# Performance work log

Measured on AMD Instinct MI355X. Metric: run time of the kernel, lower is better.

## Reference

```python
import jax, jax.numpy as jnp
import numpy as np

D_MODEL = 1024
POOL = 2048
K = 16
D_FF = 4096
N_HEADS = 16
TEMP = 1.0
EPS = 1e-5


def _ln(x, g, b):
    mu = jnp.mean(x, axis=-1, keepdims=True)
    var = jnp.mean((x - mu) ** 2, axis=-1, keepdims=True)
    return (x - mu) * jax.lax.rsqrt(var + EPS) * g + b


def setup_inputs() -> dict:
    key = jax.random.key(0)
    ks = jax.random.split(key, 12)
    s = 0.02
    return {
        "x": jax.random.normal(ks[0], (4, 1024, D_MODEL), jnp.float32),
        "w_router": s * jax.random.normal(ks[1], (D_MODEL, POOL), jnp.float32),
        "b_router": jnp.zeros((POOL,), jnp.float32),
        "firing": s * jax.random.normal(ks[2], (POOL, D_FF), jnp.float32),
        "w_pool_out": s * jax.random.normal(ks[3], (D_FF, D_MODEL), jnp.float32),
        "b_pool_out": jnp.zeros((D_MODEL,), jnp.float32),
        "w_in": s * jax.random.normal(ks[4], (D_MODEL, 3 * D_MODEL), jnp.float32),
        "b_in": jnp.zeros((3 * D_MODEL,), jnp.float32),
        "w_attn_out": s * jax.random.normal(ks[5], (D_MODEL, D_MODEL), jnp.float32),
        "b_attn_out": jnp.zeros((D_MODEL,), jnp.float32),
        "g1": jnp.ones((D_MODEL,), jnp.float32),
        "beta1": jnp.zeros((D_MODEL,), jnp.float32),
        "g2": jnp.ones((D_MODEL,), jnp.float32),
        "beta2": jnp.zeros((D_MODEL,), jnp.float32),
    }


def reference(x, w_router, b_router, firing, w_pool_out, b_pool_out,
              w_in, b_in, w_attn_out, b_attn_out, g1, beta1, g2, beta2):
    B, S, D = x.shape
    Hd = D // N_HEADS
    # --- Context router: score every neuron, select top-k, softmax weights ---
    scores = x @ w_router + b_router                      # [B,S,P]
    top_vals, top_idx = jax.lax.top_k(scores, K)          # [B,S,K]
    weights = jax.nn.softmax(top_vals / TEMP, axis=-1)    # [B,S,K]
    # --- Neuron pool: gather firing patterns, weighted combine, GELU, project ---
    patterns = firing[top_idx]                            # [B,S,K,d_ff] gather
    combined = jnp.einsum('bsk,bskf->bsf', weights, patterns)  # [B,S,d_ff]
    neuron_out = jax.nn.gelu(combined, approximate=False) @ w_pool_out + b_pool_out  # [B,S,D]
    # --- Self-attention over neuron_out (dropout inactive at eval) ---
    qkv = neuron_out @ w_in + b_in                        # [B,S,3D]
    q, k, v = jnp.split(qkv, 3, axis=-1)
    q = q.reshape(B, S, N_HEADS, Hd).transpose(0, 2, 1, 3)
    k = k.reshape(B, S, N_HEADS, Hd).transpose(0, 2, 1, 3)
    v = v.reshape(B, S, N_HEADS, Hd).transpose(0, 2, 1, 3)
    logits = jnp.einsum('bhqd,bhkd->bhqk', q, k) / jnp.sqrt(jnp.float32(Hd))
    probs = jax.nn.softmax(logits, axis=-1)
    ctx = jnp.einsum('bhqk,bhkd->bhqd', probs, v)
    ctx = ctx.transpose(0, 2, 1, 3).reshape(B, S, D)
    attn_out = ctx @ w_attn_out + b_attn_out
    # --- Residuals + norms ---
    h = _ln(x + attn_out, g1, beta1)
    out = _ln(h + neuron_out, g2, beta2)
    return out
```

## Files before the change

kernel.cpp:

```cpp
#include <hip/hip_runtime.h>
#include <math.h>

typedef __attribute__((ext_vector_type(8))) __bf16 bf16x8;
typedef __attribute__((ext_vector_type(4))) __bf16 bf16x4;
typedef __attribute__((ext_vector_type(4))) float f32x4;

#define DEV static __device__ __forceinline__

DEV float b2f(unsigned short u){ union{unsigned i; float f;} c; c.i=((unsigned)u)<<16; return c.f; }
DEV unsigned short f2b(float f){
  union{float f; unsigned u;} c; c.f=f;
  unsigned r = 0x7FFFu + ((c.u>>16)&1u);
  return (unsigned short)((c.u + r)>>16);
}
DEV unsigned pack2(float a, float b){ return (unsigned)f2b(a) | ((unsigned)f2b(b)<<16); }
DEV float gelu_exact(float x){ return 0.5f*x*(1.f+erff(x*0.70710678118654752f)); }

typedef __attribute__((address_space(1))) void gas_void;
typedef __attribute__((address_space(3))) void las_void;
DEV void gload_lds16(const unsigned short* g, unsigned short* l){
  __builtin_amdgcn_global_load_lds((const gas_void*)g, (las_void*)l, 16, 0, 0);
}

template<int N> DEV void waitcnt_vm(){
  if constexpr(N==0)      asm volatile("s_waitcnt vmcnt(0)" ::: "memory");
  else if constexpr(N==2) asm volatile("s_waitcnt vmcnt(2)" ::: "memory");
  else if constexpr(N==3) asm volatile("s_waitcnt vmcnt(3)" ::: "memory");
  else if constexpr(N==4) asm volatile("s_waitcnt vmcnt(4)" ::: "memory");
  else if constexpr(N==6) asm volatile("s_waitcnt vmcnt(6)" ::: "memory");
  else if constexpr(N==8) asm volatile("s_waitcnt vmcnt(8)" ::: "memory");
  else                    asm volatile("s_waitcnt vmcnt(0)" ::: "memory");
}

__global__ __launch_bounds__(256) void k_cast_bf16(const float* __restrict__ in,
                                                   unsigned short* __restrict__ out, long n4)
{
  long i = (long)blockIdx.x*256 + threadIdx.x;
  if (i >= n4) return;
  float4 v = ((const float4*)in)[i];
  ushort4 o; o.x=f2b(v.x); o.y=f2b(v.y); o.z=f2b(v.z); o.w=f2b(v.w);
  ((ushort4*)out)[i] = o;
}

__global__ __launch_bounds__(256) void k_transpose_cast(const float* __restrict__ in,
                                                        unsigned short* __restrict__ out,
                                                        int R, int C)
{
  __shared__ float tile[32][33];
  const int tc = blockIdx.x*32, tr = blockIdx.y*32;
  {
    const int r = threadIdx.x>>3, c4 = (threadIdx.x&7)*4;
    float4 v = *(const float4*)&in[(long)(tr+r)*C + tc+c4];
    tile[r][c4+0]=v.x; tile[r][c4+1]=v.y; tile[r][c4+2]=v.z; tile[r][c4+3]=v.w;
  }
  __syncthreads();
  {
    const int c = threadIdx.x>>3, r4 = (threadIdx.x&7)*4;
    ushort4 o;
    o.x = f2b(tile[r4+0][c]); o.y = f2b(tile[r4+1][c]);
    o.z = f2b(tile[r4+2][c]); o.w = f2b(tile[r4+3][c]);
    *(ushort4*)&out[(long)(tc+c)*R + tr+r4] = o;
  }
}

template<int WR, int WC, int FM, int FN, int OMODE>
__global__ __launch_bounds__(WR*WC*64, 2) void k_gemm_bt(
  const unsigned short* __restrict__ A, long lda, long sAb,
  const unsigned short* __restrict__ Bt, long ldb, long sBb,
  float* __restrict__ Cf, unsigned short* __restrict__ Cb, long ldc, long sCb,
  const float* __restrict__ bias, int Kiters)
{
  constexpr int WAVES = WR*WC;
  constexpr int BM = WR*FM*16, BN = WC*FN*16;
  constexpr int AR16 = BM/16, TOT16 = (BM+BN)/16;
  constexpr int UNITS = TOT16/WAVES;
  static_assert(TOT16 % WAVES == 0, "stage units must split across waves");
  __shared__ __align__(16) unsigned short S[3][TOT16*512];
  const int tid = threadIdx.x;
  const int wave = tid>>6, lane = tid&63;
  const int wr = wave/WC, wc = wave%WC;
  const int l15 = lane&15, lhi = lane>>4;
  const int lrow = lane>>2;
  const int lcol = ((lane&3) ^ ((lrow>>1)&3))*8;

  const int gx = gridDim.x;
  const int nwg = gx*gridDim.y;
  const int id = blockIdx.y*gx + blockIdx.x;
  const int sid = (id&7)*(nwg>>3) + (id>>3);
  const long bm = (long)(sid / gx)*BM, bn = (long)(sid % gx)*BN;

  const unsigned short* Ab  = A  + (long)blockIdx.z*sAb + bm*lda;
  const unsigned short* Btb = Bt + (long)blockIdx.z*sBb + bn*ldb;

  f32x4 acc[FM][FN];
  #pragma unroll
  for (int i=0;i<FM;i++)
    #pragma unroll
    for (int j=0;j<FN;j++) acc[i][j] = (f32x4){0.f,0.f,0.f,0.f};

  auto STAGE = [&](int kt, int buf){
    const long k0 = (long)kt*32;
    #pragma unroll
    for (int u=0; u<UNITS; ++u) {
      const int t = wave + u*WAVES;
      const unsigned short* g;
      if (t < AR16) g = Ab  + (long)(t*16 + lrow)*lda + k0 + lcol;
      else          g = Btb + (long)((t-AR16)*16 + lrow)*ldb + k0 + lcol;
      gload_lds16(g, &S[buf][t*512]);
    }
  };
  auto COMPUTE = [&](int buf){
    const unsigned short* Sb = S[buf];
    bf16x8 bfr[FN];
    #pragma unroll
    for (int j=0;j<FN;j++) {
      const int r = wc*(FN*16) + j*16 + l15;
      bfr[j] = *(const bf16x8*)&Sb[BM*32 + r*32 + ((lhi ^ ((r>>1)&3))*8)];
    }
    #pragma unroll
    for (int i=0;i<FM;i++) {
      const int r = wr*(FM*16) + i*16 + l15;
      bf16x8 a = *(const bf16x8*)&Sb[r*32 + ((lhi ^ ((r>>1)&3))*8)];
      #pragma unroll
      for (int j=0;j<FN;j++)
        acc[i][j] = __builtin_amdgcn_mfma_f32_16x16x32_bf16(a, bfr[j], acc[i][j], 0,0,0);
    }
  };

  STAGE(0, 0);
  if (Kiters > 1) STAGE(1, 1);
  for (int kt=0; kt<Kiters; ++kt) {
    if (kt+1 < Kiters) waitcnt_vm<UNITS>();
    else               waitcnt_vm<0>();
    __builtin_amdgcn_s_barrier();
    __builtin_amdgcn_sched_barrier(0);
    COMPUTE(kt%3);
    if (kt+2 < Kiters) STAGE(kt+2, (kt+2)%3);
  }

  #pragma unroll
  for (int i=0;i<FM;i++) {
    #pragma unroll
    for (int j=0;j<FN;j++) {
      long col = bn + wc*(FN*16) + j*16 + l15;
      float bb = bias ? bias[col] : 0.f;
      #pragma unroll
      for (int q=0;q<4;q++) {
        long row = bm + wr*(FM*16) + i*16 + lhi*4 + q;
        float v = acc[i][j][q] + bb;
        long off = (long)blockIdx.z*sCb + row*ldc + col;
        if constexpr (OMODE==0 || OMODE==2) Cf[off] = v;
        if constexpr (OMODE==1 || OMODE==2) Cb[off] = f2b(v);
      }
    }
  }
}

__global__ __launch_bounds__(256) void k_combine_bias_bf16(
    const float* __restrict__ p, long sz, const float* __restrict__ bias,
    unsigned short* __restrict__ outb)
{
  const long t = blockIdx.x;
  const int tid = threadIdx.x;
  float4 a = ((const float4*)(p + t*1024))[tid];
  float4 b = ((const float4*)(p + sz + t*1024))[tid];
  float4 bi = ((const float4*)bias)[tid];
  ushort4 o;
  o.x = f2b(a.x+b.x+bi.x); o.y = f2b(a.y+b.y+bi.y);
  o.z = f2b(a.z+b.z+bi.z); o.w = f2b(a.w+b.w+bi.w);
  ((ushort4*)(outb + t*1024))[tid] = o;
}

__global__ __launch_bounds__(256) void k_topk_softmax(const float* __restrict__ scores,
                                                      int* __restrict__ topidx,
                                                      float* __restrict__ topw)
{
  const int tid = threadIdx.x, wave = tid>>6, lane = tid&63;
  const long t = blockIdx.x;
  const float* row = scores + t*2048;
  const int base = wave*512 + lane*8;
  unsigned k0,k1,k2,k3,k4,k5,k6,k7;
  {
    float4 a = *(const float4*)(row + base);
    float4 b = *(const float4*)(row + base + 4);
    float v[8] = {a.x,a.y,a.z,a.w,b.x,b.y,b.z,b.w};
    unsigned kk[8];
    #pragma unroll
    for (int e=0;e<8;e++){
      int bi = __float_as_int(v[e]);
      unsigned u = (bi<0) ? ~(unsigned)bi : ((unsigned)bi | 0x80000000u);
      kk[e] = (u & 0xFFFFF800u) | (unsigned)(2047 - (base+e));
    }
    k0=kk[0];k1=kk[1];k2=kk[2];k3=kk[3];k4=kk[4];k5=kk[5];k6=kk[6];k7=kk[7];
  }
  #define CX(x,y) { unsigned mx = x>y?x:y, mn = x>y?y:x; x=mx; y=mn; }
  CX(k0,k1) CX(k2,k3) CX(k4,k5) CX(k6,k7)
  CX(k0,k2) CX(k1,k3) CX(k4,k6) CX(k5,k7)
  CX(k1,k2) CX(k5,k6)
  CX(k0,k4) CX(k1,k5) CX(k2,k6) CX(k3,k7)
  CX(k2,k4) CX(k3,k5)
  CX(k1,k2) CX(k3,k4) CX(k5,k6)
  #undef CX

  __shared__ unsigned wk[4][16];
  unsigned my1 = 0;
  for (int it=0; it<16; ++it){
    unsigned best = k0;
    #pragma unroll
    for (int off=1; off<64; off<<=1){
      unsigned o = __shfl_xor(best, off);
      best = o>best ? o : best;
    }
    if (lane==it) my1 = best;
    bool own = (k0==best);
    k0 = own?k1:k0; k1 = own?k2:k1; k2 = own?k3:k2; k3 = own?k4:k3;
    k4 = own?k5:k4; k5 = own?k6:k5; k6 = own?k7:k6; k7 = own?0u:k7;
  }
  if (lane < 16) wk[wave][lane] = my1;
  __syncthreads();
  if (wave == 0){
    unsigned c = wk[lane>>4][lane&15];
    unsigned my2 = 0;
    for (int it=0; it<16; ++it){
      unsigned best = c;
      #pragma unroll
      for (int off=1; off<64; off<<=1){
        unsigned o = __shfl_xor(best, off);
        best = o>best ? o : best;
      }
      if (lane==it) my2 = best;
      c = (c==best) ? 0u : c;
    }
    int idx = 2047 - (int)(my2 & 0x7FFu);
    float val = -1e30f;
    if (lane < 16) val = row[idx];
    float m0 = __shfl(val, 0);
    float e = (lane < 16) ? __expf(val - m0) : 0.f;
    float s = e;
    #pragma unroll
    for (int off=1; off<64; off<<=1) s += __shfl_xor(s, off);
    if (lane < 16){
      topw[t*16+lane]   = e/s;
      topidx[t*16+lane] = idx;
    }
  }
}

__global__ __launch_bounds__(256) void k_gather_gelu(const int* __restrict__ topidx,
                                                     const float* __restrict__ topw,
                                                     const unsigned short* __restrict__ firing,
                                                     unsigned short* __restrict__ gact)
{
  __shared__ int idx[4][16]; __shared__ float w[4][16];
  const int tid = threadIdx.x;
  const int c = blockIdx.x & 7;
  const long t0 = (long)(blockIdx.x >> 3) * 4;
  if (tid < 64) {
    int tok = tid >> 4, k = tid & 15;
    idx[tok][k] = topidx[(t0+tok)*16 + k];
    w[tok][k]   = topw[(t0+tok)*16 + k];
  }
  __syncthreads();
  const int tok = tid >> 6, lane = tid & 63;
  const int f0 = c*512 + lane*8;
  float acc[8] = {0,0,0,0,0,0,0,0};
  #pragma unroll
  for (int k=0;k<16;k++) {
    uint4 v = *(const uint4*)(firing + (long)idx[tok][k]*4096 + f0);
    const unsigned short* pu = (const unsigned short*)&v;
    float wk = w[tok][k];
    #pragma unroll
    for (int e=0;e<8;e++) acc[e] += wk * b2f(pu[e]);
  }
  float g[8];
  #pragma unroll
  for (int e=0;e<8;e++) g[e] = gelu_exact(acc[e]);
  uint4 ov;
  ov.x = pack2(g[0],g[1]); ov.y = pack2(g[2],g[3]);
  ov.z = pack2(g[4],g[5]); ov.w = pack2(g[6],g[7]);
  *(uint4*)(gact + (t0+tok)*4096 + f0) = ov;
}

__global__ __launch_bounds__(256) void k_vtrans(const unsigned short* __restrict__ qkv,
                                                unsigned short* __restrict__ vT)
{
  __shared__ unsigned short tile[64][65];
  int bh = blockIdx.y; int b = bh>>4, h = bh&15;
  long t0 = (long)blockIdx.x*64;
  const int tid = threadIdx.x;
  #pragma unroll
  for (int s=0;s<16;s++) {
    int i = tid + s*256;
    int r = i>>6, c = i&63;
    tile[r][c] = qkv[ (long)(b*1024 + t0 + r)*3072 + 2048 + h*64 + c ];
  }
  __syncthreads();
  #pragma unroll
  for (int s=0;s<16;s++) {
    int i = tid + s*256;
    int c = i>>6, r = i&63;
    vT[ (long)bh*65536 + (long)c*1024 + t0 + r ] = tile[r][c];
  }
}

__global__ __launch_bounds__(256) void k_flash_attn(
  const unsigned short* __restrict__ qkv,
  const unsigned short* __restrict__ vT,
  unsigned short* __restrict__ ctx)
{
  __shared__ __align__(16) unsigned short Ks[2][128*64];
  __shared__ __align__(16) unsigned short Vs[2][64*128];
  const int tid = threadIdx.x;
  const int wave = tid>>6, lane = tid&63;
  const int l15 = lane&15, lhi = lane>>4;
  const int bh = blockIdx.x, b = bh>>4, h = bh&15;
  const long q0 = (long)blockIdx.y*128;
  const unsigned short* Qg = qkv + ((long)b*1024 + q0)*3072 + h*64;
  const unsigned short* Kg = qkv + (long)b*1024*3072 + 1024 + h*64;
  const unsigned short* Vg = vT + (long)bh*65536;

  auto STAGE_KV = [&](int t, int s){
    const long kv0 = (long)t*128;
    const int sr = lane>>3, sc = (lane&7)^sr;
    #pragma unroll
    for (int uu=0; uu<4; ++uu){
      int u = wave + uu*4;
      gload_lds16(Kg + (kv0 + u*8 + sr)*3072 + sc*8, &Ks[s][u*512]);
    }
    const int vc = (lane&15) ^ ((wave&1)*4 + lhi);
    #pragma unroll
    for (int uu=0; uu<4; ++uu){
      int u = wave + uu*4;
      gload_lds16(Vg + (long)(u*4+lhi)*1024 + kv0 + vc*8, &Vs[s][u*512]);
    }
  };

  STAGE_KV(0, 0);

  bf16x8 qf[2][2];
  #pragma unroll
  for (int jq=0;jq<2;jq++){
    const long r = wave*32 + jq*16 + l15;
    #pragma unroll
    for (int ks=0;ks<2;ks++)
      qf[jq][ks] = *(const bf16x8*)(Qg + r*3072 + ks*32 + lhi*8);
  }
  __syncthreads();

  f32x4 acco[2][4];
  #pragma unroll
  for (int mi=0;mi<2;mi++)
    #pragma unroll
    for (int nf=0;nf<4;nf++) acco[mi][nf] = (f32x4){0.f,0.f,0.f,0.f};
  float m_run[2] = {-1e30f,-1e30f}, l_run[2] = {0.f,0.f};

  int sel = 0;
  for (int t=0; t<8; ++t) {
    if (t < 7) STAGE_KV(t+1, sel^1);
    f32x4 accs[8][2];
    #pragma unroll
    for (int fk=0;fk<8;fk++){
      accs[fk][0] = (f32x4){0.f,0.f,0.f,0.f};
      accs[fk][1] = (f32x4){0.f,0.f,0.f,0.f};
      const int r = fk*16 + l15;
      bf16x8 k0 = *(const bf16x8*)&Ks[sel][r*64 + ((lhi^(r&7))*8)];
      accs[fk][0] = __builtin_amdgcn_mfma_f32_16x16x32_bf16(k0, qf[0][0], accs[fk][0],0,0,0);
      accs[fk][1] = __builtin_amdgcn_mfma_f32_16x16x32_bf16(k0, qf[1][0], accs[fk][1],0,0,0);
      bf16x8 k1 = *(const bf16x8*)&Ks[sel][r*64 + (((4+lhi)^(r&7))*8)];
      accs[fk][0] = __builtin_amdgcn_mfma_f32_16x16x32_bf16(k1, qf[0][1], accs[fk][0],0,0,0);
      accs[fk][1] = __builtin_amdgcn_mfma_f32_16x16x32_bf16(k1, qf[1][1], accs[fk][1],0,0,0);
    }
    bf16x8 pa[2][4];
    float fsc[2];
    #pragma unroll
    for (int jq=0;jq<2;jq++){
      float mt = -1e30f;
      #pragma unroll
      for (int fk=0;fk<8;fk++)
        #pragma unroll
        for (int q=0;q<4;q++) mt = fmaxf(mt, accs[fk][jq][q]);
      mt = fmaxf(mt, __shfl_xor(mt,16));
      mt = fmaxf(mt, __shfl_xor(mt,32));
      mt *= 0.125f;
      float mnew = fmaxf(m_run[jq], mt);
      float fj = __expf(m_run[jq] - mnew);
      float ssum = 0.f;
      #pragma unroll
      for (int fk=0;fk<8;fk++)
        #pragma unroll
        for (int q=0;q<4;q++){
          float p = __expf(accs[fk][jq][q]*0.125f - mnew);
          ssum += p;
          pa[jq][fk>>1][(fk&1)*4+q] = (__bf16)p;
        }
      ssum += __shfl_xor(ssum,16);
      ssum += __shfl_xor(ssum,32);
      l_run[jq] = l_run[jq]*fj + ssum;
      m_run[jq] = mnew;
      fsc[jq] = fj;
    }
    #pragma unroll
    for (int mi=0;mi<2;mi++)
      #pragma unroll
      for (int q=0;q<4;q++){
        float fr = __shfl(fsc[mi], (lane&48)|(lhi*4+q));
        #pragma unroll
        for (int nf=0;nf<4;nf++) acco[mi][nf][q] *= fr;
      }
    #pragma unroll
    for (int kk=0;kk<4;kk++)
      #pragma unroll
      for (int nf=0;nf<4;nf++){
        const int rv = nf*16 + l15;
        const int cb = kk*4 + (lhi>>1);
        bf16x4 v0 = *(const bf16x4*)&Vs[sel][rv*128 + (( cb   ^(l15&7))*8) + (lhi&1)*4];
        bf16x4 v1 = *(const bf16x4*)&Vs[sel][rv*128 + (((cb+2)^(l15&7))*8) + (lhi&1)*4];
        bf16x8 vb = __builtin_shufflevector(v0, v1, 0,1,2,3,4,5,6,7);
        acco[0][nf] = __builtin_amdgcn_mfma_f32_16x16x32_bf16(pa[0][kk], vb, acco[0][nf],0,0,0);
        acco[1][nf] = __builtin_amdgcn_mfma_f32_16x16x32_bf16(pa[1][kk], vb, acco[1][nf],0,0,0);
      }
    __syncthreads();
    sel ^= 1;
  }

  #pragma unroll
  for (int mi=0;mi<2;mi++)
    #pragma unroll
    for (int q=0;q<4;q++){
      float lr = __shfl(l_run[mi], (lane&48)|(lhi*4+q));
      float inv = 1.f/lr;
      long row = q0 + wave*32 + mi*16 + lhi*4 + q;
      #pragma unroll
      for (int nf=0;nf<4;nf++)
        ctx[((long)b*1024 + row)*1024 + h*64 + nf*16 + l15] = f2b(acco[mi][nf][q]*inv);
    }
}

__global__ __launch_bounds__(256) void k_ln_res_fb(const float* __restrict__ a,
                                                   const unsigned short* __restrict__ b,
                                                   const float* __restrict__ g,
                                                   const float* __restrict__ be,
                                                   float* __restrict__ out)
{
  const long t = blockIdx.x;
  const int tid = threadIdx.x;
  const int wave = tid>>6, lane = tid&63;
  float4 av = ((const float4*)(a + t*1024))[tid];
  ushort4 ub = ((const ushort4*)(b + t*1024))[tid];
  float4 sv = { av.x + b2f(ub.x), av.y + b2f(ub.y),
                av.z + b2f(ub.z), av.w + b2f(ub.w) };
  float sum = sv.x+sv.y+sv.z+sv.w;
  float sq  = sv.x*sv.x + sv.y*sv.y + sv.z*sv.z + sv.w*sv.w;
  #pragma unroll
  for (int off=32; off; off>>=1){ sum += __shfl_xor(sum,off); sq += __shfl_xor(sq,off); }
  __shared__ float s1[4], s2[4];
  if (lane==0){ s1[wave]=sum; s2[wave]=sq; }
  __syncthreads();
  sum = s1[0]+s1[1]+s1[2]+s1[3];
  sq  = s2[0]+s2[1]+s2[2]+s2[3];
  float mu  = sum * (1.f/1024.f);
  float var = sq * (1.f/1024.f) - mu*mu;
  float rs  = rsqrtf(var + 1e-5f);
  float4 gv  = ((const float4*)g)[tid];
  float4 bev = ((const float4*)be)[tid];
  float4 ov = { (sv.x-mu)*rs*gv.x + bev.x,
                (sv.y-mu)*rs*gv.y + bev.y,
                (sv.z-mu)*rs*gv.z + bev.z,
                (sv.w-mu)*rs*gv.w + bev.w };
  ((float4*)(out + t*1024))[tid] = ov;
}

extern "C" void kernel_launch(void* const* d_in, const int* in_sizes, int n_in,
                              void* d_out, int out_size, void* d_ws, size_t ws_size,
                              hipStream_t stream)
{
  const float* x        = (const float*)d_in[0];
  const float* w_router = (const float*)d_in[1];
  const float* b_router = (const float*)d_in[2];
  const float* firing   = (const float*)d_in[3];
  const float* w_pool   = (const float*)d_in[4];
  const float* b_pool   = (const float*)d_in[5];
  const float* w_in     = (const float*)d_in[6];
  const float* b_in     = (const float*)d_in[7];
  const float* w_ao     = (const float*)d_in[8];
  const float* b_ao     = (const float*)d_in[9];
  const float* g1       = (const float*)d_in[10];
  const float* be1      = (const float*)d_in[11];
  const float* g2       = (const float*)d_in[12];
  const float* be2      = (const float*)d_in[13];
  float* out = (float*)d_out;
  char* ws = (char*)d_ws;

  unsigned short* xb    = (unsigned short*)(ws + 0);
  unsigned short* wrT   = (unsigned short*)(ws + 8388608);
  unsigned short* firb  = (unsigned short*)(ws + 12582912);
  unsigned short* wpoT  = (unsigned short*)(ws + 29360128);
  unsigned short* winT  = (unsigned short*)(ws + 37748736);
  unsigned short* waoT  = (unsigned short*)(ws + 44040192);
  float*  scores        = (float*)(ws + 46137344);
  unsigned short* gact  = (unsigned short*)(ws + 46137344);
  int*    topi          = (int*)(ws + 79691776);
  float*  topw          = (float*)(ws + 79953920);
  unsigned short* attnb = (unsigned short*)(ws + 80216064);
  unsigned short* neub  = (unsigned short*)(ws + 96993280);
  unsigned short* qkvb  = (unsigned short*)(ws + 105381888);
  unsigned short* vT    = (unsigned short*)(ws + 130547712);
  unsigned short* ctx   = (unsigned short*)(ws + 138936320);
  float*  hbuf          = (float*)(ws + 147324928);
  float*  poolp         = (float*)(ws + 130547712);

  if (ws_size < 164102144u) return;

  k_cast_bf16<<<4096, 256, 0, stream>>>(x, xb, 4096L*1024/4);
  k_cast_bf16<<<8192, 256, 0, stream>>>(firing, firb, 2048L*4096/4);
  k_transpose_cast<<<dim3(2048/32, 1024/32), 256, 0, stream>>>(w_router, wrT, 1024, 2048);
  k_transpose_cast<<<dim3(1024/32, 4096/32), 256, 0, stream>>>(w_pool,   wpoT, 4096, 1024);
  k_transpose_cast<<<dim3(3072/32, 1024/32), 256, 0, stream>>>(w_in,     winT, 1024, 3072);
  k_transpose_cast<<<dim3(1024/32, 1024/32), 256, 0, stream>>>(w_ao,     waoT, 1024, 1024);

  k_gemm_bt<2,2,4,4,0><<<dim3(16,32,1),256,0,stream>>>(xb,1024,0, wrT,1024,0,
        scores,nullptr,2048,0, b_router, 32);
  k_topk_softmax<<<4096,256,0,stream>>>(scores, topi, topw);
  k_gather_gelu<<<8192,256,0,stream>>>(topi, topw, firb, gact);

  k_gemm_bt<2,2,4,4,0><<<dim3(8,32,2),256,0,stream>>>(gact,4096,2048, wpoT,4096,2048,
        poolp,nullptr,1024,4194304, nullptr, 64);
  k_combine_bias_bf16<<<4096,256,0,stream>>>(poolp, 4194304, b_pool, neub);

  k_gemm_bt<2,2,4,4,1><<<dim3(24,32,1),256,0,stream>>>(neub,1024,0, winT,1024,0,
        nullptr,qkvb,3072,0, b_in, 32);

  k_vtrans<<<dim3(16,64),256,0,stream>>>(qkvb, vT);
  k_flash_attn<<<dim3(64,8),256,0,stream>>>(qkvb, vT, ctx);

  k_gemm_bt<2,2,4,2,1><<<dim3(16,32,1),256,0,stream>>>(ctx,1024,0, waoT,1024,0,
        nullptr,attnb,1024,0, b_ao, 32);

  k_ln_res_fb<<<4096,256,0,stream>>>(x, attnb, g1, be1, hbuf);
  k_ln_res_fb<<<4096,256,0,stream>>>(hbuf, neub, g2, be2, out);
}
```

Measured before the change: 275.1 us.

## Use 8 waves per flash-attention block with lazy softmax rescaling

Flash attention now runs 512 threads per block, so each wave owns 16 query rows instead of 32, which halves per-thread accumulators and register pressure and raises occupancy. K/V staging is split across 8 waves. Online softmax now skips the max update and accumulator rescale unless the new tile max exceeds the running max by more than 8 (in the scaled log domain). This is the FlashAttention-4 style conditional rescale, which stays exact after final normalisation but allows unnormalised probabilities up to about e^8 in bf16/fp32. Each K/V tile loaded into LDS is now reused by fewer query rows per wave, though still by 128 query rows per block.

After: 271.8 us. About the same (-1.2%).

```diff
diff --git a/kernel.cpp b/kernel.cpp
--- a/kernel.cpp
+++ b/kernel.cpp
@@ -303,7 +303,7 @@
   }
 }
 
-__global__ __launch_bounds__(256) void k_flash_attn(
+__global__ __launch_bounds__(512, 4) void k_flash_attn(
   const unsigned short* __restrict__ qkv,
   const unsigned short* __restrict__ vT,
   unsigned short* __restrict__ ctx)
@@ -323,90 +323,79 @@
     const long kv0 = (long)t*128;
     const int sr = lane>>3, sc = (lane&7)^sr;
     #pragma unroll
-    for (int uu=0; uu<4; ++uu){
-      int u = wave + uu*4;
+    for (int uu=0; uu<2; ++uu){
+      int u = wave + uu*8;
       gload_lds16(Kg + (kv0 + u*8 + sr)*3072 + sc*8, &Ks[s][u*512]);
     }
     const int vc = (lane&15) ^ ((wave&1)*4 + lhi);
     #pragma unroll
-    for (int uu=0; uu<4; ++uu){
-      int u = wave + uu*4;
+    for (int uu=0; uu<2; ++uu){
+      int u = wave + uu*8;
       gload_lds16(Vg + (long)(u*4+lhi)*1024 + kv0 + vc*8, &Vs[s][u*512]);
     }
   };
 
   STAGE_KV(0, 0);
 
-  bf16x8 qf[2][2];
-  #pragma unroll
-  for (int jq=0;jq<2;jq++){
-    const long r = wave*32 + jq*16 + l15;
-    #pragma unroll
-    for (int ks=0;ks<2;ks++)
-      qf[jq][ks] = *(const bf16x8*)(Qg + r*3072 + ks*32 + lhi*8);
+  bf16x8 qf[2];
+  {
+    const long r = wave*16 + l15;
+    qf[0] = *(const bf16x8*)(Qg + r*3072 + lhi*8);
+    qf[1] = *(const bf16x8*)(Qg + r*3072 + 32 + lhi*8);
   }
   __syncthreads();
 
-  f32x4 acco[2][4];
-  #pragma unroll
-  for (int mi=0;mi<2;mi++)
-    #pragma unroll
-    for (int nf=0;nf<4;nf++) acco[mi][nf] = (f32x4){0.f,0.f,0.f,0.f};
-  float m_run[2] = {-1e30f,-1e30f}, l_run[2] = {0.f,0.f};
+  f32x4 acco[4];
+  #pragma unroll
+  for (int nf=0;nf<4;nf++) acco[nf] = (f32x4){0.f,0.f,0.f,0.f};
+  float m_run = -1e30f, l_run = 0.f;
 
   int sel = 0;
   for (int t=0; t<8; ++t) {
     if (t < 7) STAGE_KV(t+1, sel^1);
-    f32x4 accs[8][2];
+    f32x4 accs[8];
     #pragma unroll
     for (int fk=0;fk<8;fk++){
-      accs[fk][0] = (f32x4){0.f,0.f,0.f,0.f};
-      accs[fk][1] = (f32x4){0.f,0.f,0.f,0.f};
+      accs[fk] = (f32x4){0.f,0.f,0.f,0.f};
       const int r = fk*16 + l15;
       bf16x8 k0 = *(const bf16x8*)&Ks[sel][r*64 + ((lhi^(r&7))*8)];
-      accs[fk][0] = __builtin_amdgcn_mfma_f32_16x16x32_bf16(k0, qf[0][0], accs[fk][0],0,0,0);
-      accs[fk][1] = __builtin_amdgcn_mfma_f32_16x16x32_bf16(k0, qf[1][0], accs[fk][1],0,0,0);
+      accs[fk] = __builtin_amdgcn_mfma_f32_16x16x32_bf16(k0, qf[0], accs[fk],0,0,0);
       bf16x8 k1 = *(const bf16x8*)&Ks[sel][r*64 + (((4+lhi)^(r&7))*8)];
-      accs[fk][0] = __builtin_amdgcn_mfma_f32_16x16x32_bf16(k1, qf[0][1], accs[fk][0],0,0,0);
-      accs[fk][1] = __builtin_amdgcn_mfma_f32_16x16x32_bf16(k1, qf[1][1], accs[fk][1],0,0,0);
-    }
-    bf16x8 pa[2][4];
-    float fsc[2];
-    #pragma unroll
-    for (int jq=0;jq<2;jq++){
-      float mt = -1e30f;
-      #pragma unroll
-      for (int fk=0;fk<8;fk++)
+      accs[fk] = __builtin_amdgcn_mfma_f32_16x16x32_bf16(k1, qf[1], accs[fk],0,0,0);
+    }
+    float mt = -1e30f;
+    #pragma unroll
+    for (int fk=0;fk<8;fk++)
+      #pragma unroll
+      for (int q=0;q<4;q++) mt = fmaxf(mt, accs[fk][q]);
+    mt = fmaxf(mt, __shfl_xor(mt,16));
+    mt = fmaxf(mt, __shfl_xor(mt,32));
+    mt *= 0.125f;
+    if (!__all(mt <= m_run + 8.f)) {
+      float mnew = fmaxf(m_run, mt);
+      float fj = __expf(m_run - mnew);
+      l_run *= fj;
+      #pragma unroll
+      for (int q=0;q<4;q++){
+        float fr = __shfl(fj, (lane&48)|(lhi*4+q));
         #pragma unroll
-        for (int q=0;q<4;q++) mt = fmaxf(mt, accs[fk][jq][q]);
-      mt = fmaxf(mt, __shfl_xor(mt,16));
-      mt = fmaxf(mt, __shfl_xor(mt,32));
-      mt *= 0.125f;
-      float mnew = fmaxf(m_run[jq], mt);
-      float fj = __expf(m_run[jq] - mnew);
-      float ssum = 0.f;
-      #pragma unroll
-      for (int fk=0;fk<8;fk++)
-        #pragma unroll
-        for (int q=0;q<4;q++){
-          float p = __expf(accs[fk][jq][q]*0.125f - mnew);
-          ssum += p;
-          pa[jq][fk>>1][(fk&1)*4+q] = (__bf16)p;
-        }
-      ssum += __shfl_xor(ssum,16);
-      ssum += __shfl_xor(ssum,32);
-      l_run[jq] = l_run[jq]*fj + ssum;
-      m_run[jq] = mnew;
-      fsc[jq] = fj;
-    }
-    #pragma unroll
-    for (int mi=0;mi<2;mi++)
+        for (int nf=0;nf<4;nf++) acco[nf][q] *= fr;
+      }
+      m_run = mnew;
+    }
+    bf16x8 pa[4];
+    float ssum = 0.f;
+    #pragma unroll
+    for (int fk=0;fk<8;fk++)
       #pragma unroll
       for (int q=0;q<4;q++){
-        float fr = __shfl(fsc[mi], (lane&48)|(lhi*4+q));
-        #pragma unroll
-        for (int nf=0;nf<4;nf++) acco[mi][nf][q] *= fr;
+        float p = __expf(accs[fk][q]*0.125f - m_run);
+        ssum += p;
+        pa[fk>>1][(fk&1)*4+q] = (__bf16)p;
       }
+    ssum += __shfl_xor(ssum,16);
+    ssum += __shfl_xor(ssum,32);
+    l_run += ssum;
     #pragma unroll
     for (int kk=0;kk<4;kk++)
       #pragma unroll
@@ -416,24 +405,21 @@
         bf16x4 v0 = *(const bf16x4*)&Vs[sel][rv*128 + (( cb   ^(l15&7))*8) + (lhi&1)*4];
         bf16x4 v1 = *(const bf16x4*)&Vs[sel][rv*128 + (((cb+2)^(l15&7))*8) + (lhi&1)*4];
         bf16x8 vb = __builtin_shufflevector(v0, v1, 0,1,2,3,4,5,6,7);
-        acco[0][nf] = __builtin_amdgcn_mfma_f32_16x16x32_bf16(pa[0][kk], vb, acco[0][nf],0,0,0);
-        acco[1][nf] = __builtin_amdgcn_mfma_f32_16x16x32_bf16(pa[1][kk], vb, acco[1][nf],0,0,0);
+        acco[nf] = __builtin_amdgcn_mfma_f32_16x16x32_bf16(pa[kk], vb, acco[nf],0,0,0);
       }
     __syncthreads();
     sel ^= 1;
   }
 
   #pragma unroll
-  for (int mi=0;mi<2;mi++)
-    #pragma unroll
-    for (int q=0;q<4;q++){
-      float lr = __shfl(l_run[mi], (lane&48)|(lhi*4+q));
-      float inv = 1.f/lr;
-      long row = q0 + wave*32 + mi*16 + lhi*4 + q;
-      #pragma unroll
-      for (int nf=0;nf<4;nf++)
-        ctx[((long)b*1024 + row)*1024 + h*64 + nf*16 + l15] = f2b(acco[mi][nf][q]*inv);
-    }
+  for (int q=0;q<4;q++){
+    float lr = __shfl(l_run, (lane&48)|(lhi*4+q));
+    float inv = 1.f/lr;
+    long row = q0 + wave*16 + lhi*4 + q;
+    #pragma unroll
+    for (int nf=0;nf<4;nf++)
+      ctx[((long)b*1024 + row)*1024 + h*64 + nf*16 + l15] = f2b(acco[nf][q]*inv);
+  }
 }
 
 __global__ __launch_bounds__(256) void k_ln_res_fb(const float* __restrict__ a,
@@ -531,7 +517,7 @@
         nullptr,qkvb,3072,0, b_in, 32);
 
   k_vtrans<<<dim3(16,64),256,0,stream>>>(qkvb, vT);
-  k_flash_attn<<<dim3(64,8),256,0,stream>>>(qkvb, vT, ctx);
+  k_flash_attn<<<dim3(64,8),512,0,stream>>>(qkvb, vT, ctx);
 
   k_gemm_bt<2,2,4,2,1><<<dim3(16,32,1),256,0,stream>>>(ctx,1024,0, waoT,1024,0,
         nullptr,attnb,1024,0, b_ao, 32);
```
